# Kernel tuning notes

Hardware: AMD Instinct MI355X
Metric: run time of the kernel (lower is better)

The kernel has to match this reference:

```python
import jax, jax.numpy as jnp
import numpy as np

N_ATOMS = 10000
N_EDGES = 200000
L_MAX = 2
K_L = [32, 24, 16]  # k_max_l = n_element_channels * n_max_l

# (l1, l2, L) in the original loop order (l1 outer, l2 inner, L ascending)
PAIRS = [(0,0,0),(0,1,1),(0,2,2),
         (1,0,1),(1,1,0),(1,1,1),(1,1,2),(1,2,1),(1,2,2),
         (2,0,2),(2,1,1),(2,1,2),(2,2,0),(2,2,1),(2,2,2)]
# concatenated input width -> k_max_l[L] per (L, sigma) channel
LIN = {'0_1': (72, 32), '1_1': (80, 24), '1_m1': (40, 24), '2_1': (72, 16), '2_m1': (32, 16)}


def setup_inputs() -> dict:
    key = jax.random.key(0)
    it = iter(jax.random.split(key, 64))
    def nrm(shape):
        return jax.random.normal(next(it), shape, dtype=jnp.float32)
    inp = {}
    for l in range(L_MAX + 1):
        inp['rb%d' % l] = nrm((N_EDGES, K_L[l]))           # radial basis per l
    for l in range(L_MAX + 1):
        inp['sh%d' % l] = nrm((N_EDGES, 2*l+1, 1))         # spherical harmonics per l
    inp['emb'] = nrm((N_ATOMS, 1, K_L[0]))                 # initial center embedding
    for l in range(L_MAX + 1):
        inp['f%d' % l] = nrm((N_ATOMS, 2*l+1, K_L[l]))     # nu=1 equivariant features
    for (l1, l2, L) in PAIRS:
        inp['cg_%d_%d_%d' % (l1, l2, L)] = nrm(((2*l1+1)*(2*l2+1), 2*L+1))
    for LS, (fin, fout) in LIN.items():
        inp['W_' + LS] = nrm((fin, fout)) / np.float32(np.sqrt(fin))
        inp['b_' + LS] = nrm((fout,)) * 0.01
    inp['centers'] = jax.random.randint(next(it), (N_EDGES,), 0, N_ATOMS)
    inp['neighbors'] = jax.random.randint(next(it), (N_EDGES,), 0, N_ATOMS)
    inp['n_atoms'] = N_ATOMS
    return inp


def _normalize(x, dims):
    # Normalizer(dims): RMS normalization over the given dims
    return x * jax.lax.rsqrt(jnp.mean(x * x, axis=dims, keepdims=True) + 1e-12)


def _forward(floats, centers, neighbors, n_atoms):
    (rb0, rb1, rb2, sh0, sh1, sh2, emb, f0, f1, f2,
     cg_0_0_0, cg_0_1_1, cg_0_2_2, cg_1_0_1, cg_1_1_0, cg_1_1_1, cg_1_1_2,
     cg_1_2_1, cg_1_2_2, cg_2_0_2, cg_2_1_1, cg_2_1_2, cg_2_2_0, cg_2_2_1,
     cg_2_2_2, W_0_1, b_0_1, W_1_1, b_1_1, W_1_m1, b_1_m1, W_2_1, b_2_1,
     W_2_m1, b_2_m1) = floats
    rb = [rb0, rb1, rb2]; sh = [sh0, sh1, sh2]; feats = [f0, f1, f2]
    cgs = {'0_0_0': cg_0_0_0, '0_1_1': cg_0_1_1, '0_2_2': cg_0_2_2,
           '1_0_1': cg_1_0_1, '1_1_0': cg_1_1_0, '1_1_1': cg_1_1_1,
           '1_1_2': cg_1_1_2, '1_2_1': cg_1_2_1, '1_2_2': cg_1_2_2,
           '2_0_2': cg_2_0_2, '2_1_1': cg_2_1_1, '2_1_2': cg_2_1_2,
           '2_2_0': cg_2_2_0, '2_2_1': cg_2_2_1, '2_2_2': cg_2_2_2}
    lin = {'0_1': (W_0_1, b_0_1), '1_1': (W_1_1, b_1_1), '1_m1': (W_1_m1, b_1_m1),
           '2_1': (W_2_1, b_2_1), '2_m1': (W_2_m1, b_2_m1)}

    # ---- InvariantMessagePasser: density_l = scatter_add over centers of
    #      sh_l * rb_l * emb[neighbors]
    emb_n = emb[neighbors]                                       # [E, 1, k0]
    densities = []
    for l in range(L_MAX + 1):
        msg = sh[l] * rb[l][:, None, :] * emb_n[:, :, :K_L[l]]   # [E, 2l+1, k_l]
        densities.append(jax.ops.segment_sum(msg, centers, num_segments=n_atoms))

    # ---- EquivariantMessagePasser
    ve = [sh[l] * rb[l][:, None, :] for l in range(L_MAX + 1)]   # vector expansion [E,2l+1,k_l]
    fn = [feats[l][neighbors] for l in range(L_MAX + 1)]         # gathered neighbor feats
    results = {}
    for (l1, l2, L) in PAIRS:
        S = (-1) ** (l1 + l2 + L)
        k = min(K_L[l1], K_L[l2])
        t1 = ve[l1][:, :, :k]                                    # [E, 2l1+1, k]
        t2 = fn[l2][:, :, :k]                                    # [E, 2l2+1, k]
        cg = cgs['%d_%d_%d' % (l1, l2, L)].reshape(2*l1+1, 2*l2+1, 2*L+1)
        # fused outer product + CG contraction -> [E, 2L+1, k]
        res = jnp.einsum('eak,ebk,abM->eMk', t1, t2, cg)
        pooled = jax.ops.segment_sum(res, centers, num_segments=n_atoms)
        LS = '%d_%s' % (L, 'm1' if S < 0 else '1')
        results.setdefault(LS, []).append(pooled)

    outs = {}
    for LS, (W, b) in lin.items():
        x = jnp.concatenate(results[LS], axis=2)                 # [n_atoms, 2L+1, size_LS]
        x = _normalize(x, (0, 1))
        x = jnp.einsum('amf,fk->amk', x, W) + b
        outs[LS] = _normalize(x, (0, 1, 2))

    return (densities[0], densities[1], densities[2],
            outs['0_1'], outs['1_1'], outs['1_m1'], outs['2_1'], outs['2_m1'])


def reference(rb0, rb1, rb2, sh0, sh1, sh2, emb, f0, f1, f2,
              cg_0_0_0, cg_0_1_1, cg_0_2_2, cg_1_0_1, cg_1_1_0, cg_1_1_1,
              cg_1_1_2, cg_1_2_1, cg_1_2_2, cg_2_0_2, cg_2_1_1, cg_2_1_2,
              cg_2_2_0, cg_2_2_1, cg_2_2_2, W_0_1, b_0_1, W_1_1, b_1_1,
              W_1_m1, b_1_m1, W_2_1, b_2_1, W_2_m1, b_2_m1,
              centers, neighbors, n_atoms):
    floats = (rb0, rb1, rb2, sh0, sh1, sh2, emb, f0, f1, f2,
              cg_0_0_0, cg_0_1_1, cg_0_2_2, cg_1_0_1, cg_1_1_0, cg_1_1_1,
              cg_1_1_2, cg_1_2_1, cg_1_2_2, cg_2_0_2, cg_2_1_1, cg_2_1_2,
              cg_2_2_0, cg_2_2_1, cg_2_2_2, W_0_1, b_0_1, W_1_1, b_1_1,
              W_1_m1, b_1_m1, W_2_1, b_2_1, W_2_m1, b_2_m1)
    return _forward(floats, centers, neighbors, n_atoms)
```

## Files before the change

### kernel.cpp

```cpp
#include <hip/hip_runtime.h>
#include <hip/hip_bf16.h>

typedef __hip_bfloat16 bf16;

#define N_ATOMS 10000
#define N_EDGES 200000

#define SCG   0
#define SINV  616
#define SS1P  1024
#define SS2P  19968
#define SWS2  20288
#define SINTS 20352
#define IFLAG  0
#define ICOUNT 16
#define IOFFS  10016
#define ICURS  20032
#define IELIST 30032
#define INTS_END_SMALL 230032
#define INTS_END_BIG   430032
#define SXACC (SINTS + INTS_END_BIG)
#define BIG_FLOATS (SXACC + 952*N_ATOMS)

#define O0 0
#define O1 320000
#define O2 1040000
#define OY 1840000

__device__ __forceinline__ float b2f(bf16 x){ return __bfloat162float(x); }
__device__ __forceinline__ bf16  f2b(float x){ return __float2bfloat16(x); }

__device__ __forceinline__ float ldv(const float* p, int i){ return p[i]; }
__device__ __forceinline__ float ldv(const bf16*  p, int i){ return b2f(p[i]); }
__device__ __forceinline__ void  stv(float* p, int i, float v){ p[i] = v; }
__device__ __forceinline__ void  stv(bf16*  p, int i, float v){ p[i] = f2b(v); }

template<typename T> __device__ __forceinline__ int dtid();
template<> __device__ __forceinline__ int dtid<bf16>(){ return 0; }
template<> __device__ __forceinline__ int dtid<float>(){ return 1; }

struct Ptrs15 { const void* p[15]; };
struct LinP   { const void* W[5]; const void* B[5]; };

__constant__ int c_cg_sizes[15] = {1,9,25,9,9,27,45,45,75,25,45,75,25,75,125};
__constant__ int c_fin[5]   = {72,80,40,72,32};
__constant__ int c_kout[5]  = {32,24,24,16,16};
__constant__ int c_yoff[5]  = {OY+0, OY+320000, OY+1040000, OY+1760000, OY+2560000};
__constant__ int c_numel[5] = {320000,720000,720000,800000,800000};
__constant__ int c_cum[6]   = {0,32,104,176,256,336};
__constant__ int c_xb[5]    = {0,72,312,432,792};
__constant__ int c_Ms[5]    = {1,3,3,5,5};

__global__ void k_probe(const unsigned short* rb0u, const unsigned short* embu,
                        int* flag) {
  int lane = threadIdx.x;
  int bad = 0;
  for (int i = lane; i < 256; i += 64) {
    unsigned u1 = ((unsigned)rb0u[2*i]) << 16;
    unsigned u2 = ((unsigned)embu[2*i]) << 16;
    float v1 = __uint_as_float(u1);
    float v2 = __uint_as_float(u2);
    if (!(fabsf(v1) < 1e9f) || !(fabsf(v2) < 1e9f)) bad = 1;
  }
  unsigned long long any = __ballot(bad);
  if (lane == 0) flag[0] = (any != 0ULL) ? 1 : 0;
}

__global__ void k_zero(float* wsf, int* wsi) {
  int i = blockIdx.x*blockDim.x + threadIdx.x;
  if (i < N_ATOMS) wsi[ICOUNT + i] = 0;
  int j = i - N_ATOMS;
  if (j >= 0 && j < N_ATOMS) wsi[ICURS + j] = 0;
  j -= N_ATOMS;
  if (j >= 0 && j < 18944) wsf[SS1P + j] = 0.f;
  j -= 18944;
  if (j >= 0 && j < 325) wsf[SS2P + j] = 0.f;
}

template<typename T>
__global__ void k_cg(Ptrs15 cg, float* wsf, const int* flag) {
  if (flag[0] != dtid<T>()) return;
  int i = blockIdx.x*blockDim.x + threadIdx.x;
  if (i >= 615) return;
  int s = 0, off = i;
  while (off >= c_cg_sizes[s]) { off -= c_cg_sizes[s]; ++s; }
  wsf[SCG + i] = ldv((const T*)cg.p[s], off);
}

__global__ void k_hist(const int* __restrict__ centers, int* __restrict__ counts) {
  int e = blockIdx.x*blockDim.x + threadIdx.x;
  if (e < N_EDGES) atomicAdd(&counts[centers[e]], 1);
}

__global__ void k_scan(const int* __restrict__ counts, int* __restrict__ offs) {
  __shared__ int part[1024];
  int t = threadIdx.x;
  int base = t*10;
  int s = 0;
  for (int i = 0; i < 10; ++i) { int idx = base+i; if (idx < N_ATOMS) s += counts[idx]; }
  part[t] = s;
  __syncthreads();
  for (int d = 1; d < 1024; d <<= 1) {
    int v = part[t];
    int add = (t >= d) ? part[t-d] : 0;
    __syncthreads();
    part[t] = v + add;
    __syncthreads();
  }
  int run = (t == 0) ? 0 : part[t-1];
  for (int i = 0; i < 10; ++i) {
    int idx = base+i;
    if (idx < N_ATOMS) { offs[idx] = run; run += counts[idx]; }
  }
  if (t == 1023) offs[N_ATOMS] = part[1023];
}

__global__ void k_scatter(const int* __restrict__ centers, const int* __restrict__ offs,
                          int* __restrict__ cursors, int* __restrict__ elist) {
  int e = blockIdx.x*blockDim.x + threadIdx.x;
  if (e < N_EDGES) {
    int c = centers[e];
    int p = atomicAdd(&cursors[c], 1);
    elist[offs[c] + p] = e;
  }
}

__global__ void k_scatter2(const int* __restrict__ centers, const int* __restrict__ neighbors,
                           const int* __restrict__ offs, int* __restrict__ cursors,
                           int2* __restrict__ elist2) {
  int e = blockIdx.x*blockDim.x + threadIdx.x;
  if (e < N_EDGES) {
    int c = centers[e];
    int p = atomicAdd(&cursors[c], 1);
    elist2[offs[c] + p] = make_int2(e, neighbors[e]);
  }
}

template<typename T, int MODE>
__global__ __launch_bounds__(256) void k_main(
    const T* __restrict__ rb0, const T* __restrict__ rb1, const T* __restrict__ rb2,
    const T* __restrict__ sh0, const T* __restrict__ sh1, const T* __restrict__ sh2,
    const T* __restrict__ emb, const T* __restrict__ f0, const T* __restrict__ f1,
    const T* __restrict__ f2, const int* __restrict__ neighbors,
    const int* __restrict__ offs, const int* __restrict__ elist,
    const float* __restrict__ cgf, float* __restrict__ s1p,
    const float* __restrict__ inv, float* __restrict__ s2p,
    float* __restrict__ xout, LinP lp, T* __restrict__ out,
    const int* __restrict__ flag)
{
  if (flag[0] != dtid<T>()) return;
  int lane = threadIdx.x & 63;
  int wv   = threadIdx.x >> 6;
  int a = blockIdx.x;
  int beg = offs[a];
  int cnt = offs[a+1] - beg;
  int k32 = lane & 31, e2 = lane >> 5;
  int k16 = lane & 15, e4 = lane >> 4;
  const int2* el2 = (const int2*)elist;
  int ab = a & 63;

  __shared__ float L[952];
  __shared__ float red[4][5];

  float acc[20];
  #pragma unroll
  for (int i = 0; i < 20; ++i) acc[i] = 0.f;

  if (wv == 0) {
    const float* C000 = cgf + 0;
    const float* C011 = cgf + 1;
    const float* C101 = cgf + 35;
    const float* C110 = cgf + 44;
    const float* C111 = cgf + 53;
    const float* C112 = cgf + 80;
    for (int base = 0; base < cnt; base += 2) {
      int idx = base + e2;
      if (idx < cnt) {
        int e, n;
        if constexpr (MODE == 0) { int2 en = el2[beg + idx]; e = en.x; n = en.y; }
        else { e = elist[beg + idx]; n = neighbors[e]; }
        float s0 = ldv(sh0, e);
        float s1a0 = ldv(sh1, e*3+0), s1a1 = ldv(sh1, e*3+1), s1a2 = ldv(sh1, e*3+2);
        float rb0k = ldv(rb0, e*32 + k32);
        float ek   = ldv(emb, n*32 + k32);
        float f0k  = ldv(f0,  n*32 + k32);
        float ve0 = s0 * rb0k;
        acc[0] = fmaf(ve0, ek, acc[0]);
        acc[4] = fmaf(C000[0]*ve0, f0k, acc[4]);
        if (k32 < 24) {
          float rb1k = ldv(rb1, e*24 + k32);
          float f1k0 = ldv(f1, n*72 + k32);
          float f1k1 = ldv(f1, n*72 + 24 + k32);
          float f1k2 = ldv(f1, n*72 + 48 + k32);
          float rbek = rb1k * ek;
          acc[1] = fmaf(s1a0, rbek, acc[1]);
          acc[2] = fmaf(s1a1, rbek, acc[2]);
          acc[3] = fmaf(s1a2, rbek, acc[3]);
          #pragma unroll
          for (int bb = 0; bb < 3; ++bb) {
            float fb = (bb==0)?f1k0:(bb==1)?f1k1:f1k2;
            float p = ve0 * fb;
            #pragma unroll
            for (int M = 0; M < 3; ++M) acc[5+M] = fmaf(p, C011[bb*3+M], acc[5+M]);
          }
          float g3 = rb1k * f0k;
          #pragma unroll
          for (int aa = 0; aa < 3; ++aa) {
            float sa = (aa==0)?s1a0:(aa==1)?s1a1:s1a2;
            float p = g3 * sa;
            #pragma unroll
            for (int M = 0; M < 3; ++M) acc[8+M] = fmaf(p, C101[aa*3+M], acc[8+M]);
          }
          #pragma unroll
          for (int aa = 0; aa < 3; ++aa) {
            float sa = rb1k * ((aa==0)?s1a0:(aa==1)?s1a1:s1a2);
            #pragma unroll
            for (int bb = 0; bb < 3; ++bb) {
              float fb = (bb==0)?f1k0:(bb==1)?f1k1:f1k2;
              float p = sa * fb;
              int q = aa*3+bb;
              acc[11] = fmaf(p, C110[q], acc[11]);
              #pragma unroll
              for (int M = 0; M < 3; ++M) acc[12+M] = fmaf(p, C111[q*3+M], acc[12+M]);
              #pragma unroll
              for (int M = 0; M < 5; ++M) acc[15+M] = fmaf(p, C112[q*5+M], acc[15+M]);
            }
          }
        }
      }
    }
    #pragma unroll
    for (int i = 0; i < 20; ++i) acc[i] += __shfl_xor(acc[i], 32);
  } else if (wv == 1) {
    const float* C022 = cgf + 10;
    const float* C121 = cgf + 125;
    const float* C122 = cgf + 170;
    for (int base = 0; base < cnt; base += 4) {
      int idx = base + e4;
      if (idx < cnt) {
        int e, n;
        if constexpr (MODE == 0) { int2 en = el2[beg + idx]; e = en.x; n = en.y; }
        else { e = elist[beg + idx]; n = neighbors[e]; }
        float s0 = ldv(sh0, e);
        float s1a[3];
        #pragma unroll
        for (int m = 0; m < 3; ++m) s1a[m] = ldv(sh1, e*3+m);
        float s2a[5];
        #pragma unroll
        for (int m = 0; m < 5; ++m) s2a[m] = ldv(sh2, e*5+m);
        float rb0k = ldv(rb0, e*32 + k16);
        float rb1k = ldv(rb1, e*24 + k16);
        float rb2k = ldv(rb2, e*16 + k16);
        float ek   = ldv(emb, n*32 + k16);
        float f2k[5];
        #pragma unroll
        for (int b = 0; b < 5; ++b) f2k[b] = ldv(f2, n*80 + b*16 + k16);
        float re = rb2k * ek;
        #pragma unroll
        for (int m = 0; m < 5; ++m) acc[m] = fmaf(s2a[m], re, acc[m]);
        float ve0 = s0 * rb0k;
        #pragma unroll
        for (int bb = 0; bb < 5; ++bb) {
          float p = ve0 * f2k[bb];
          #pragma unroll
          for (int M = 0; M < 5; ++M) acc[5+M] = fmaf(p, C022[bb*5+M], acc[5+M]);
        }
        #pragma unroll
        for (int aa = 0; aa < 3; ++aa) {
          float sa = rb1k * s1a[aa];
          #pragma unroll
          for (int bb = 0; bb < 5; ++bb) {
            float p = sa * f2k[bb];
            int q = aa*5+bb;
            #pragma unroll
            for (int M = 0; M < 3; ++M) acc[10+M] = fmaf(p, C121[q*3+M], acc[10+M]);
            #pragma unroll
            for (int M = 0; M < 5; ++M) acc[13+M] = fmaf(p, C122[q*5+M], acc[13+M]);
          }
        }
      }
    }
    #pragma unroll
    for (int i = 0; i < 18; ++i) {
      acc[i] += __shfl_xor(acc[i], 16);
      acc[i] += __shfl_xor(acc[i], 32);
    }
  } else if (wv == 2) {
    const float* C202 = cgf + 245;
    const float* C211 = cgf + 270;
    const float* C212 = cgf + 315;
    for (int base = 0; base < cnt; base += 4) {
      int idx = base + e4;
      if (idx < cnt) {
        int e, n;
        if constexpr (MODE == 0) { int2 en = el2[beg + idx]; e = en.x; n = en.y; }
        else { e = elist[beg + idx]; n = neighbors[e]; }
        float s2a[5];
        #pragma unroll
        for (int m = 0; m < 5; ++m) s2a[m] = ldv(sh2, e*5+m);
        float rb2k = ldv(rb2, e*16 + k16);
        float f0k  = ldv(f0,  n*32 + k16);
        float f1k[3];
        #pragma unroll
        for (int b = 0; b < 3; ++b) f1k[b] = ldv(f1, n*72 + b*24 + k16);
        float g9 = rb2k * f0k;
        #pragma unroll
        for (int aa = 0; aa < 5; ++aa) {
          float p = g9 * s2a[aa];
          #pragma unroll
          for (int M = 0; M < 5; ++M) acc[0+M] = fmaf(p, C202[aa*5+M], acc[0+M]);
        }
        #pragma unroll
        for (int aa = 0; aa < 5; ++aa) {
          float sa = rb2k * s2a[aa];
          #pragma unroll
          for (int bb = 0; bb < 3; ++bb) {
            float p = sa * f1k[bb];
            int q = aa*3+bb;
            #pragma unroll
            for (int M = 0; M < 3; ++M) acc[5+M] = fmaf(p, C211[q*3+M], acc[5+M]);
            #pragma unroll
            for (int M = 0; M < 5; ++M) acc[8+M] = fmaf(p, C212[q*5+M], acc[8+M]);
          }
        }
      }
    }
    #pragma unroll
    for (int i = 0; i < 13; ++i) {
      acc[i] += __shfl_xor(acc[i], 16);
      acc[i] += __shfl_xor(acc[i], 32);
    }
  } else {
    const float* C220 = cgf + 390;
    const float* C221 = cgf + 415;
    const float* C222 = cgf + 490;
    for (int base = 0; base < cnt; base += 4) {
      int idx = base + e4;
      if (idx < cnt) {
        int e, n;
        if constexpr (MODE == 0) { int2 en = el2[beg + idx]; e = en.x; n = en.y; }
        else { e = elist[beg + idx]; n = neighbors[e]; }
        float s2a[5];
        #pragma unroll
        for (int m = 0; m < 5; ++m) s2a[m] = ldv(sh2, e*5+m);
        float rb2k = ldv(rb2, e*16 + k16);
        float f2k[5];
        #pragma unroll
        for (int b = 0; b < 5; ++b) f2k[b] = ldv(f2, n*80 + b*16 + k16);
        #pragma unroll
        for (int aa = 0; aa < 5; ++aa) {
          float sa = rb2k * s2a[aa];
          #pragma unroll
          for (int bb = 0; bb < 5; ++bb) {
            float p = sa * f2k[bb];
            int q = aa*5+bb;
            acc[0] = fmaf(p, C220[q], acc[0]);
            #pragma unroll
            for (int M = 0; M < 3; ++M) acc[1+M] = fmaf(p, C221[q*3+M], acc[1+M]);
            #pragma unroll
            for (int M = 0; M < 5; ++M) acc[4+M] = fmaf(p, C222[q*5+M], acc[4+M]);
          }
        }
      }
    }
    #pragma unroll
    for (int i = 0; i < 9; ++i) {
      acc[i] += __shfl_xor(acc[i], 16);
      acc[i] += __shfl_xor(acc[i], 32);
    }
  }

  if constexpr (MODE != 2) {
    if (wv == 0) {
      if (lane < 32) {
        stv(out, O0 + a*32 + k32, acc[0]);
        atomicAdd(&s1p[(0+k32)*64+ab], acc[4]*acc[4]);
        if (k32 < 24) {
          #pragma unroll
          for (int m = 0; m < 3; ++m) stv(out, O1 + a*72 + m*24 + k32, acc[1+m]);
          atomicAdd(&s1p[(32+k32)*64+ab], acc[11]*acc[11]);
          float q;
          q = acc[5]*acc[5]+acc[6]*acc[6]+acc[7]*acc[7];
          atomicAdd(&s1p[(72+k32)*64+ab], q);
          q = acc[8]*acc[8]+acc[9]*acc[9]+acc[10]*acc[10];
          atomicAdd(&s1p[(96+k32)*64+ab], q);
          q = acc[12]*acc[12]+acc[13]*acc[13]+acc[14]*acc[14];
          atomicAdd(&s1p[(152+k32)*64+ab], q);
          q = acc[15]*acc[15]+acc[16]*acc[16]+acc[17]*acc[17]
            + acc[18]*acc[18]+acc[19]*acc[19];
          atomicAdd(&s1p[(208+k32)*64+ab], q);
        }
      }
    } else if (wv == 1) {
      if (lane < 16) {
        #pragma unroll
        for (int m = 0; m < 5; ++m) stv(out, O2 + a*80 + m*16 + k16, acc[m]);
        float q;
        q = acc[5]*acc[5]+acc[6]*acc[6]+acc[7]*acc[7]+acc[8]*acc[8]+acc[9]*acc[9];
        atomicAdd(&s1p[(192+k16)*64+ab], q);
        q = acc[10]*acc[10]+acc[11]*acc[11]+acc[12]*acc[12];
        atomicAdd(&s1p[(120+k16)*64+ab], q);
        q = acc[13]*acc[13]+acc[14]*acc[14]+acc[15]*acc[15]
          + acc[16]*acc[16]+acc[17]*acc[17];
        atomicAdd(&s1p[(264+k16)*64+ab], q);
      }
    } else if (wv == 2) {
      if (lane < 16) {
        float q;
        q = acc[0]*acc[0]+acc[1]*acc[1]+acc[2]*acc[2]+acc[3]*acc[3]+acc[4]*acc[4];
        atomicAdd(&s1p[(232+k16)*64+ab], q);
        q = acc[5]*acc[5]+acc[6]*acc[6]+acc[7]*acc[7];
        atomicAdd(&s1p[(136+k16)*64+ab], q);
        q = acc[8]*acc[8]+acc[9]*acc[9]+acc[10]*acc[10]
          + acc[11]*acc[11]+acc[12]*acc[12];
        atomicAdd(&s1p[(280+k16)*64+ab], q);
      }
    } else {
      if (lane < 16) {
        atomicAdd(&s1p[(56+k16)*64+ab], acc[0]*acc[0]);
        float q;
        q = acc[1]*acc[1]+acc[2]*acc[2]+acc[3]*acc[3];
        atomicAdd(&s1p[(176+k16)*64+ab], q);
        q = acc[4]*acc[4]+acc[5]*acc[5]+acc[6]*acc[6]
          + acc[7]*acc[7]+acc[8]*acc[8];
        atomicAdd(&s1p[(248+k16)*64+ab], q);
      }
    }
  }

  if constexpr (MODE == 0) {
    float* xg = xout + a*952;
    if (wv == 0) {
      if (lane < 32) {
        xg[k32] = acc[4];
        if (k32 < 24) {
          xg[32+k32] = acc[11];
          #pragma unroll
          for (int M = 0; M < 3; ++M) xg[72+M*80+k32]     = acc[5+M];
          #pragma unroll
          for (int M = 0; M < 3; ++M) xg[72+M*80+24+k32]  = acc[8+M];
          #pragma unroll
          for (int M = 0; M < 3; ++M) xg[312+M*40+k32]    = acc[12+M];
          #pragma unroll
          for (int M = 0; M < 5; ++M) xg[432+M*72+16+k32] = acc[15+M];
        }
      }
    } else if (wv == 1) {
      if (lane < 16) {
        #pragma unroll
        for (int M = 0; M < 5; ++M) xg[432+M*72+k16]    = acc[5+M];
        #pragma unroll
        for (int M = 0; M < 3; ++M) xg[72+M*80+48+k16]  = acc[10+M];
        #pragma unroll
        for (int M = 0; M < 5; ++M) xg[792+M*32+k16]    = acc[13+M];
      }
    } else if (wv == 2) {
      if (lane < 16) {
        #pragma unroll
        for (int M = 0; M < 5; ++M) xg[432+M*72+40+k16] = acc[0+M];
        #pragma unroll
        for (int M = 0; M < 3; ++M) xg[72+M*80+64+k16]  = acc[5+M];
        #pragma unroll
        for (int M = 0; M < 5; ++M) xg[792+M*32+16+k16] = acc[8+M];
      }
    } else {
      if (lane < 16) {
        xg[56+k16] = acc[0];
        #pragma unroll
        for (int M = 0; M < 3; ++M) xg[312+M*40+24+k16] = acc[1+M];
        #pragma unroll
        for (int M = 0; M < 5; ++M) xg[432+M*72+56+k16] = acc[4+M];
      }
    }
  }

  if constexpr (MODE == 2) {
    if (wv == 0) {
      if (lane < 32) {
        L[k32] = acc[4]*inv[k32];
        if (k32 < 24) {
          L[32+k32] = acc[11]*inv[32+k32];
          #pragma unroll
          for (int M = 0; M < 3; ++M) L[72+M*80+k32]     = acc[5+M]*inv[72+k32];
          #pragma unroll
          for (int M = 0; M < 3; ++M) L[72+M*80+24+k32]  = acc[8+M]*inv[96+k32];
          #pragma unroll
          for (int M = 0; M < 3; ++M) L[312+M*40+k32]    = acc[12+M]*inv[152+k32];
          #pragma unroll
          for (int M = 0; M < 5; ++M) L[432+M*72+16+k32] = acc[15+M]*inv[208+k32];
        }
      }
    } else if (wv == 1) {
      if (lane < 16) {
        #pragma unroll
        for (int M = 0; M < 5; ++M) L[432+M*72+k16]    = acc[5+M]*inv[192+k16];
        #pragma unroll
        for (int M = 0; M < 3; ++M) L[72+M*80+48+k16]  = acc[10+M]*inv[120+k16];
        #pragma unroll
        for (int M = 0; M < 5; ++M) L[792+M*32+k16]    = acc[13+M]*inv[264+k16];
      }
    } else if (wv == 2) {
      if (lane < 16) {
        #pragma unroll
        for (int M = 0; M < 5; ++M) L[432+M*72+40+k16] = acc[0+M]*inv[232+k16];
        #pragma unroll
        for (int M = 0; M < 3; ++M) L[72+M*80+64+k16]  = acc[5+M]*inv[136+k16];
        #pragma unroll
        for (int M = 0; M < 5; ++M) L[792+M*32+16+k16] = acc[8+M]*inv[280+k16];
      }
    } else {
      if (lane < 16) {
        L[56+k16] = acc[0]*inv[56+k16];
        #pragma unroll
        for (int M = 0; M < 3; ++M) L[312+M*40+24+k16] = acc[1+M]*inv[176+k16];
        #pragma unroll
        for (int M = 0; M < 5; ++M) L[432+M*72+56+k16] = acc[4+M]*inv[248+k16];
      }
    }
    __syncthreads();
    int t = threadIdx.x;
    float y2[5] = {0.f,0.f,0.f,0.f,0.f};
    for (int tau = t; tau < 336; tau += 256) {
      int ls = 0;
      while (tau >= c_cum[ls+1]) ++ls;
      int rem = tau - c_cum[ls];
      int kn = c_kout[ls], fin = c_fin[ls];
      int M = rem / kn, ko = rem - M*kn;
      const T* W = (const T*)lp.W[ls];
      float y = ldv((const T*)lp.B[ls], ko);
      const float* xv = &L[c_xb[ls] + M*fin];
      for (int f = 0; f < fin; ++f) y = fmaf(xv[f], ldv(W, f*kn+ko), y);
      stv(out, c_yoff[ls] + (a*c_Ms[ls] + M)*kn + ko, y);
      y2[ls] += y*y;
    }
    #pragma unroll
    for (int i = 0; i < 5; ++i) {
      y2[i] += __shfl_xor(y2[i], 1);  y2[i] += __shfl_xor(y2[i], 2);
      y2[i] += __shfl_xor(y2[i], 4);  y2[i] += __shfl_xor(y2[i], 8);
      y2[i] += __shfl_xor(y2[i], 16); y2[i] += __shfl_xor(y2[i], 32);
    }
    if (lane == 0) {
      #pragma unroll
      for (int i = 0; i < 5; ++i) red[wv][i] = y2[i];
    }
    __syncthreads();
    if (t == 0) {
      #pragma unroll
      for (int i = 0; i < 5; ++i)
        atomicAdd(&s2p[i*64 + ab], red[0][i]+red[1][i]+red[2][i]+red[3][i]);
    }
  }
}

template<typename T>
__global__ __launch_bounds__(256) void k_lin(
    const float* __restrict__ xg, const float* __restrict__ inv,
    LinP lp, T* __restrict__ out, float* __restrict__ s2p,
    const int* __restrict__ flag)
{
  if (flag[0] != dtid<T>()) return;
  int a = blockIdx.x;
  int t = threadIdx.x;
  __shared__ float L[952];
  for (int i = t; i < 952; i += 256) {
    int ch;
    if      (i < 72)  ch = i;
    else if (i < 312) ch = 72  + (i-72)  % 80;
    else if (i < 432) ch = 152 + (i-312) % 40;
    else if (i < 792) ch = 192 + (i-432) % 72;
    else              ch = 264 + (i-792) % 32;
    L[i] = xg[a*952 + i] * inv[ch];
  }
  __syncthreads();
  float y2[5] = {0.f,0.f,0.f,0.f,0.f};
  for (int tau = t; tau < 336; tau += 256) {
    int ls = 0;
    while (tau >= c_cum[ls+1]) ++ls;
    int rem = tau - c_cum[ls];
    int kn = c_kout[ls], fin = c_fin[ls];
    int M = rem / kn, ko = rem - M*kn;
    const T* W = (const T*)lp.W[ls];
    float y = ldv((const T*)lp.B[ls], ko);
    const float* xv = &L[c_xb[ls] + M*fin];
    for (int f = 0; f < fin; ++f) y = fmaf(xv[f], ldv(W, f*kn+ko), y);
    stv(out, c_yoff[ls] + (a*c_Ms[ls] + M)*kn + ko, y);
    y2[ls] += y*y;
  }
  __shared__ float red[4][5];
  #pragma unroll
  for (int i = 0; i < 5; ++i) {
    y2[i] += __shfl_xor(y2[i], 1);  y2[i] += __shfl_xor(y2[i], 2);
    y2[i] += __shfl_xor(y2[i], 4);  y2[i] += __shfl_xor(y2[i], 8);
    y2[i] += __shfl_xor(y2[i], 16); y2[i] += __shfl_xor(y2[i], 32);
  }
  if ((t & 63) == 0) {
    #pragma unroll
    for (int i = 0; i < 5; ++i) red[t>>6][i] = y2[i];
  }
  __syncthreads();
  if (t == 0) {
    #pragma unroll
    for (int i = 0; i < 5; ++i)
      atomicAdd(&s2p[i*64 + (a & 63)], red[0][i]+red[1][i]+red[2][i]+red[3][i]);
  }
}

__global__ void k_red1(const float* __restrict__ s1p, float* __restrict__ inv) {
  int ch = blockIdx.x, lane = threadIdx.x;
  float v = s1p[ch*64 + lane];
  v += __shfl_xor(v, 1);  v += __shfl_xor(v, 2);  v += __shfl_xor(v, 4);
  v += __shfl_xor(v, 8);  v += __shfl_xor(v, 16); v += __shfl_xor(v, 32);
  if (lane == 0) {
    float rows = (ch < 72) ? 10000.f : (ch < 192) ? 30000.f : 50000.f;
    inv[ch] = rsqrtf(v/rows + 1e-12f);
  }
}

__global__ void k_red2(const float* __restrict__ s2p, float* __restrict__ ws2) {
  int ls = blockIdx.x, lane = threadIdx.x;
  float v = s2p[ls*64 + lane];
  v += __shfl_xor(v, 1);  v += __shfl_xor(v, 2);  v += __shfl_xor(v, 4);
  v += __shfl_xor(v, 8);  v += __shfl_xor(v, 16); v += __shfl_xor(v, 32);
  if (lane == 0) ws2[ls] = v;
}

template<typename T>
__global__ void k_scale(const float* __restrict__ ws2, T* __restrict__ out,
                        const int* __restrict__ flag) {
  if (flag[0] != dtid<T>()) return;
  int i = blockIdx.x*blockDim.x + threadIdx.x;
  if (i >= 3360000) return;
  int ls = (i < 320000) ? 0 : (i < 1040000) ? 1 : (i < 1760000) ? 2 : (i < 2560000) ? 3 : 4;
  float scale = rsqrtf(ws2[ls] / (float)c_numel[ls] + 1e-12f);
  stv(out, OY + i, ldv((const T*)out, OY + i) * scale);
}

template<typename T>
static void launch_chain(void* const* d_in, T* out, float* wsf, int* wsi,
                         Ptrs15 cg, LinP lp, bool big, hipStream_t stream) {
  const T* rb0 = (const T*)d_in[0];
  const T* rb1 = (const T*)d_in[1];
  const T* rb2 = (const T*)d_in[2];
  const T* sh0 = (const T*)d_in[3];
  const T* sh1 = (const T*)d_in[4];
  const T* sh2 = (const T*)d_in[5];
  const T* emb = (const T*)d_in[6];
  const T* f0  = (const T*)d_in[7];
  const T* f1  = (const T*)d_in[8];
  const T* f2  = (const T*)d_in[9];
  const int* neighbors = (const int*)d_in[36];
  const int* flag = wsi + IFLAG;

  k_cg<T><<<3, 256, 0, stream>>>(cg, wsf, flag);
  if (big) {
    k_main<T,0><<<N_ATOMS, 256, 0, stream>>>(rb0, rb1, rb2, sh0, sh1, sh2, emb, f0, f1, f2,
        neighbors, wsi+IOFFS, wsi+IELIST, wsf+SCG, wsf+SS1P, nullptr, nullptr,
        wsf+SXACC, lp, out, flag);
    k_red1<<<296, 64, 0, stream>>>(wsf+SS1P, wsf+SINV);
    k_lin<T><<<N_ATOMS, 256, 0, stream>>>(wsf+SXACC, wsf+SINV, lp, out, wsf+SS2P, flag);
  } else {
    k_main<T,1><<<N_ATOMS, 256, 0, stream>>>(rb0, rb1, rb2, sh0, sh1, sh2, emb, f0, f1, f2,
        neighbors, wsi+IOFFS, wsi+IELIST, wsf+SCG, wsf+SS1P, nullptr, nullptr,
        nullptr, lp, out, flag);
    k_red1<<<296, 64, 0, stream>>>(wsf+SS1P, wsf+SINV);
    k_main<T,2><<<N_ATOMS, 256, 0, stream>>>(rb0, rb1, rb2, sh0, sh1, sh2, emb, f0, f1, f2,
        neighbors, wsi+IOFFS, wsi+IELIST, wsf+SCG, nullptr, wsf+SINV, wsf+SS2P,
        nullptr, lp, out, flag);
  }
  k_red2<<<5, 64, 0, stream>>>(wsf+SS2P, wsf+SWS2);
  k_scale<T><<<(3360000+255)/256, 256, 0, stream>>>(wsf+SWS2, out, flag);
}

extern "C" void kernel_launch(void* const* d_in, const int* in_sizes, int n_in,
                              void* d_out, int out_size, void* d_ws, size_t ws_size,
                              hipStream_t stream) {
  float* wsf = (float*)d_ws;
  int*   wsi = (int*)(wsf + SINTS);
  const int* centers   = (const int*)d_in[35];
  const int* neighbors = (const int*)d_in[36];
  bool big = ws_size >= (size_t)BIG_FLOATS * 4;

  Ptrs15 cg;
  for (int i = 0; i < 15; ++i) cg.p[i] = d_in[10+i];
  LinP lp;
  lp.W[0] = d_in[25]; lp.B[0] = d_in[26];
  lp.W[1] = d_in[27]; lp.B[1] = d_in[28];
  lp.W[2] = d_in[29]; lp.B[2] = d_in[30];
  lp.W[3] = d_in[31]; lp.B[3] = d_in[32];
  lp.W[4] = d_in[33]; lp.B[4] = d_in[34];

  k_probe<<<1, 64, 0, stream>>>((const unsigned short*)d_in[0],
                                (const unsigned short*)d_in[6], wsi + IFLAG);
  k_zero<<<154, 256, 0, stream>>>(wsf, wsi);
  k_hist<<<(N_EDGES+255)/256, 256, 0, stream>>>(centers, wsi+ICOUNT);
  k_scan<<<1, 1024, 0, stream>>>(wsi+ICOUNT, wsi+IOFFS);
  if (big) {
    k_scatter2<<<(N_EDGES+255)/256, 256, 0, stream>>>(centers, neighbors, wsi+IOFFS,
                                                      wsi+ICURS, (int2*)(wsi+IELIST));
  } else {
    k_scatter<<<(N_EDGES+255)/256, 256, 0, stream>>>(centers, wsi+IOFFS, wsi+ICURS, wsi+IELIST);
  }

  launch_chain<bf16 >(d_in, (bf16*)d_out,  wsf, wsi, cg, lp, big, stream);
  launch_chain<float>(d_in, (float*)d_out, wsf, wsi, cg, lp, big, stream);
}
```

Before: 517.4 us.

## Stage edge lists in LDS, fuse probe into zero kernel, skip unused dtype chain

Merges the dtype probe into the zeroing kernel, which removes one launch. Each block now loads chunks of 256 (edge, neighbor) pairs into shared memory once, and all four waves read from there instead of each gathering them from global memory. Wave 0 unrolls two edges per iteration with masked weights, and MODE 0 writes its output through LDS with coalesced float4 stores. On the host, the input byte size decides which dtype chain to launch, so the unused chain's launches are skipped. The risk is that the host-side dtype detection depends on in_sizes being filled in.

Result: no change. 511.5 us (-1.1%).

```diff
diff --git a/kernel.cpp b/kernel.cpp
--- a/kernel.cpp
+++ b/kernel.cpp
@@ -51,22 +51,21 @@
 __constant__ int c_xb[5]    = {0,72,312,432,792};
 __constant__ int c_Ms[5]    = {1,3,3,5,5};
 
-__global__ void k_probe(const unsigned short* rb0u, const unsigned short* embu,
-                        int* flag) {
-  int lane = threadIdx.x;
-  int bad = 0;
-  for (int i = lane; i < 256; i += 64) {
-    unsigned u1 = ((unsigned)rb0u[2*i]) << 16;
-    unsigned u2 = ((unsigned)embu[2*i]) << 16;
-    float v1 = __uint_as_float(u1);
-    float v2 = __uint_as_float(u2);
-    if (!(fabsf(v1) < 1e9f) || !(fabsf(v2) < 1e9f)) bad = 1;
-  }
-  unsigned long long any = __ballot(bad);
-  if (lane == 0) flag[0] = (any != 0ULL) ? 1 : 0;
-}
-
-__global__ void k_zero(float* wsf, int* wsi) {
+__global__ void k_zero(float* wsf, int* wsi,
+                       const unsigned short* rb0u, const unsigned short* embu) {
+  if (blockIdx.x == 0 && threadIdx.x < 64) {
+    int lane = threadIdx.x;
+    int bad = 0;
+    for (int i = lane; i < 256; i += 64) {
+      unsigned u1 = ((unsigned)rb0u[2*i]) << 16;
+      unsigned u2 = ((unsigned)embu[2*i]) << 16;
+      float v1 = __uint_as_float(u1);
+      float v2 = __uint_as_float(u2);
+      if (!(fabsf(v1) < 1e9f) || !(fabsf(v2) < 1e9f)) bad = 1;
+    }
+    unsigned long long any = __ballot(bad);
+    if (lane == 0) wsi[IFLAG] = (any != 0ULL) ? 1 : 0;
+  }
   int i = blockIdx.x*blockDim.x + threadIdx.x;
   if (i < N_ATOMS) wsi[ICOUNT + i] = 0;
   int j = i - N_ATOMS;
@@ -151,6 +150,7 @@
   if (flag[0] != dtid<T>()) return;
   int lane = threadIdx.x & 63;
   int wv   = threadIdx.x >> 6;
+  int tix  = threadIdx.x;
   int a = blockIdx.x;
   int beg = offs[a];
   int cnt = offs[a+1] - beg;
@@ -159,210 +159,230 @@
   const int2* el2 = (const int2*)elist;
   int ab = a & 63;
 
-  __shared__ float L[952];
+  __shared__ int2 sel[256];
+  __shared__ __align__(16) float L[952];
   __shared__ float red[4][5];
 
   float acc[20];
   #pragma unroll
   for (int i = 0; i < 20; ++i) acc[i] = 0.f;
 
-  if (wv == 0) {
-    const float* C000 = cgf + 0;
-    const float* C011 = cgf + 1;
-    const float* C101 = cgf + 35;
-    const float* C110 = cgf + 44;
-    const float* C111 = cgf + 53;
-    const float* C112 = cgf + 80;
-    for (int base = 0; base < cnt; base += 2) {
-      int idx = base + e2;
-      if (idx < cnt) {
-        int e, n;
-        if constexpr (MODE == 0) { int2 en = el2[beg + idx]; e = en.x; n = en.y; }
-        else { e = elist[beg + idx]; n = neighbors[e]; }
-        float s0 = ldv(sh0, e);
-        float s1a0 = ldv(sh1, e*3+0), s1a1 = ldv(sh1, e*3+1), s1a2 = ldv(sh1, e*3+2);
-        float rb0k = ldv(rb0, e*32 + k32);
-        float ek   = ldv(emb, n*32 + k32);
-        float f0k  = ldv(f0,  n*32 + k32);
-        float ve0 = s0 * rb0k;
-        acc[0] = fmaf(ve0, ek, acc[0]);
-        acc[4] = fmaf(C000[0]*ve0, f0k, acc[4]);
-        if (k32 < 24) {
-          float rb1k = ldv(rb1, e*24 + k32);
-          float f1k0 = ldv(f1, n*72 + k32);
-          float f1k1 = ldv(f1, n*72 + 24 + k32);
-          float f1k2 = ldv(f1, n*72 + 48 + k32);
-          float rbek = rb1k * ek;
-          acc[1] = fmaf(s1a0, rbek, acc[1]);
-          acc[2] = fmaf(s1a1, rbek, acc[2]);
-          acc[3] = fmaf(s1a2, rbek, acc[3]);
-          #pragma unroll
-          for (int bb = 0; bb < 3; ++bb) {
-            float fb = (bb==0)?f1k0:(bb==1)?f1k1:f1k2;
-            float p = ve0 * fb;
-            #pragma unroll
-            for (int M = 0; M < 3; ++M) acc[5+M] = fmaf(p, C011[bb*3+M], acc[5+M]);
-          }
-          float g3 = rb1k * f0k;
-          #pragma unroll
-          for (int aa = 0; aa < 3; ++aa) {
-            float sa = (aa==0)?s1a0:(aa==1)?s1a1:s1a2;
-            float p = g3 * sa;
-            #pragma unroll
-            for (int M = 0; M < 3; ++M) acc[8+M] = fmaf(p, C101[aa*3+M], acc[8+M]);
-          }
-          #pragma unroll
-          for (int aa = 0; aa < 3; ++aa) {
-            float sa = rb1k * ((aa==0)?s1a0:(aa==1)?s1a1:s1a2);
+  for (int cbase = 0; cbase < cnt; cbase += 256) {
+    int nch = cnt - cbase; if (nch > 256) nch = 256;
+    __syncthreads();
+    if (tix < nch) {
+      if constexpr (MODE == 0) {
+        sel[tix] = el2[beg + cbase + tix];
+      } else {
+        int e = elist[beg + cbase + tix];
+        sel[tix] = make_int2(e, neighbors[e]);
+      }
+    }
+    __syncthreads();
+
+    if (wv == 0) {
+      const float* C000 = cgf + 0;
+      const float* C011 = cgf + 1;
+      const float* C101 = cgf + 35;
+      const float* C110 = cgf + 44;
+      const float* C111 = cgf + 53;
+      const float* C112 = cgf + 80;
+      for (int base = 0; base < nch; base += 4) {
+        #pragma unroll
+        for (int u = 0; u < 2; ++u) {
+          int idx = base + 2*u + e2;
+          float w = (idx < nch) ? 1.f : 0.f;
+          int ic  = (idx < nch) ? idx : (nch - 1);
+          int2 en = sel[ic];
+          int e = en.x, n = en.y;
+          float s0 = ldv(sh0, e);
+          float s1a0 = ldv(sh1, e*3+0), s1a1 = ldv(sh1, e*3+1), s1a2 = ldv(sh1, e*3+2);
+          float rb0k = ldv(rb0, e*32 + k32) * w;
+          float ek   = ldv(emb, n*32 + k32);
+          float f0k  = ldv(f0,  n*32 + k32);
+          float ve0 = s0 * rb0k;
+          acc[0] = fmaf(ve0, ek, acc[0]);
+          acc[4] = fmaf(C000[0]*ve0, f0k, acc[4]);
+          if (k32 < 24) {
+            float rb1k = ldv(rb1, e*24 + k32) * w;
+            float f1k0 = ldv(f1, n*72 + k32);
+            float f1k1 = ldv(f1, n*72 + 24 + k32);
+            float f1k2 = ldv(f1, n*72 + 48 + k32);
+            float rbek = rb1k * ek;
+            acc[1] = fmaf(s1a0, rbek, acc[1]);
+            acc[2] = fmaf(s1a1, rbek, acc[2]);
+            acc[3] = fmaf(s1a2, rbek, acc[3]);
             #pragma unroll
             for (int bb = 0; bb < 3; ++bb) {
               float fb = (bb==0)?f1k0:(bb==1)?f1k1:f1k2;
-              float p = sa * fb;
-              int q = aa*3+bb;
-              acc[11] = fmaf(p, C110[q], acc[11]);
-              #pragma unroll
-              for (int M = 0; M < 3; ++M) acc[12+M] = fmaf(p, C111[q*3+M], acc[12+M]);
-              #pragma unroll
-              for (int M = 0; M < 5; ++M) acc[15+M] = fmaf(p, C112[q*5+M], acc[15+M]);
+              float p = ve0 * fb;
+              #pragma unroll
+              for (int M = 0; M < 3; ++M) acc[5+M] = fmaf(p, C011[bb*3+M], acc[5+M]);
+            }
+            float g3 = rb1k * f0k;
+            #pragma unroll
+            for (int aa = 0; aa < 3; ++aa) {
+              float sa = (aa==0)?s1a0:(aa==1)?s1a1:s1a2;
+              float p = g3 * sa;
+              #pragma unroll
+              for (int M = 0; M < 3; ++M) acc[8+M] = fmaf(p, C101[aa*3+M], acc[8+M]);
+            }
+            #pragma unroll
+            for (int aa = 0; aa < 3; ++aa) {
+              float sa = rb1k * ((aa==0)?s1a0:(aa==1)?s1a1:s1a2);
+              #pragma unroll
+              for (int bb = 0; bb < 3; ++bb) {
+                float fb = (bb==0)?f1k0:(bb==1)?f1k1:f1k2;
+                float p = sa * fb;
+                int q = aa*3+bb;
+                acc[11] = fmaf(p, C110[q], acc[11]);
+                #pragma unroll
+                for (int M = 0; M < 3; ++M) acc[12+M] = fmaf(p, C111[q*3+M], acc[12+M]);
+                #pragma unroll
+                for (int M = 0; M < 5; ++M) acc[15+M] = fmaf(p, C112[q*5+M], acc[15+M]);
+              }
             }
           }
         }
       }
-    }
+    } else if (wv == 1) {
+      const float* C022 = cgf + 10;
+      const float* C121 = cgf + 125;
+      const float* C122 = cgf + 170;
+      for (int base = 0; base < nch; base += 4) {
+        int idx = base + e4;
+        if (idx < nch) {
+          int2 en = sel[idx];
+          int e = en.x, n = en.y;
+          float s0 = ldv(sh0, e);
+          float s1a[3];
+          #pragma unroll
+          for (int m = 0; m < 3; ++m) s1a[m] = ldv(sh1, e*3+m);
+          float s2a[5];
+          #pragma unroll
+          for (int m = 0; m < 5; ++m) s2a[m] = ldv(sh2, e*5+m);
+          float rb0k = ldv(rb0, e*32 + k16);
+          float rb1k = ldv(rb1, e*24 + k16);
+          float rb2k = ldv(rb2, e*16 + k16);
+          float ek   = ldv(emb, n*32 + k16);
+          float f2k[5];
+          #pragma unroll
+          for (int b = 0; b < 5; ++b) f2k[b] = ldv(f2, n*80 + b*16 + k16);
+          float re = rb2k * ek;
+          #pragma unroll
+          for (int m = 0; m < 5; ++m) acc[m] = fmaf(s2a[m], re, acc[m]);
+          float ve0 = s0 * rb0k;
+          #pragma unroll
+          for (int bb = 0; bb < 5; ++bb) {
+            float p = ve0 * f2k[bb];
+            #pragma unroll
+            for (int M = 0; M < 5; ++M) acc[5+M] = fmaf(p, C022[bb*5+M], acc[5+M]);
+          }
+          #pragma unroll
+          for (int aa = 0; aa < 3; ++aa) {
+            float sa = rb1k * s1a[aa];
+            #pragma unroll
+            for (int bb = 0; bb < 5; ++bb) {
+              float p = sa * f2k[bb];
+              int q = aa*5+bb;
+              #pragma unroll
+              for (int M = 0; M < 3; ++M) acc[10+M] = fmaf(p, C121[q*3+M], acc[10+M]);
+              #pragma unroll
+              for (int M = 0; M < 5; ++M) acc[13+M] = fmaf(p, C122[q*5+M], acc[13+M]);
+            }
+          }
+        }
+      }
+    } else if (wv == 2) {
+      const float* C202 = cgf + 245;
+      const float* C211 = cgf + 270;
+      const float* C212 = cgf + 315;
+      for (int base = 0; base < nch; base += 4) {
+        int idx = base + e4;
+        if (idx < nch) {
+          int2 en = sel[idx];
+          int e = en.x, n = en.y;
+          float s2a[5];
+          #pragma unroll
+          for (int m = 0; m < 5; ++m) s2a[m] = ldv(sh2, e*5+m);
+          float rb2k = ldv(rb2, e*16 + k16);
+          float f0k  = ldv(f0,  n*32 + k16);
+          float f1k[3];
+          #pragma unroll
+          for (int b = 0; b < 3; ++b) f1k[b] = ldv(f1, n*72 + b*24 + k16);
+          float g9 = rb2k * f0k;
+          #pragma unroll
+          for (int aa = 0; aa < 5; ++aa) {
+            float p = g9 * s2a[aa];
+            #pragma unroll
+            for (int M = 0; M < 5; ++M) acc[0+M] = fmaf(p, C202[aa*5+M], acc[0+M]);
+          }
+          #pragma unroll
+          for (int aa = 0; aa < 5; ++aa) {
+            float sa = rb2k * s2a[aa];
+            #pragma unroll
+            for (int bb = 0; bb < 3; ++bb) {
+              float p = sa * f1k[bb];
+              int q = aa*3+bb;
+              #pragma unroll
+              for (int M = 0; M < 3; ++M) acc[5+M] = fmaf(p, C211[q*3+M], acc[5+M]);
+              #pragma unroll
+              for (int M = 0; M < 5; ++M) acc[8+M] = fmaf(p, C212[q*5+M], acc[8+M]);
+            }
+          }
+        }
+      }
+    } else {
+      const float* C220 = cgf + 390;
+      const float* C221 = cgf + 415;
+      const float* C222 = cgf + 490;
+      for (int base = 0; base < nch; base += 4) {
+        int idx = base + e4;
+        if (idx < nch) {
+          int2 en = sel[idx];
+          int e = en.x, n = en.y;
+          float s2a[5];
+          #pragma unroll
+          for (int m = 0; m < 5; ++m) s2a[m] = ldv(sh2, e*5+m);
+          float rb2k = ldv(rb2, e*16 + k16);
+          float f2k[5];
+          #pragma unroll
+          for (int b = 0; b < 5; ++b) f2k[b] = ldv(f2, n*80 + b*16 + k16);
+          #pragma unroll
+          for (int aa = 0; aa < 5; ++aa) {
+            float sa = rb2k * s2a[aa];
+            #pragma unroll
+            for (int bb = 0; bb < 5; ++bb) {
+              float p = sa * f2k[bb];
+              int q = aa*5+bb;
+              acc[0] = fmaf(p, C220[q], acc[0]);
+              #pragma unroll
+              for (int M = 0; M < 3; ++M) acc[1+M] = fmaf(p, C221[q*3+M], acc[1+M]);
+              #pragma unroll
+              for (int M = 0; M < 5; ++M) acc[4+M] = fmaf(p, C222[q*5+M], acc[4+M]);
+            }
+          }
+        }
+      }
+    }
+  }
+
+  if (wv == 0) {
     #pragma unroll
     for (int i = 0; i < 20; ++i) acc[i] += __shfl_xor(acc[i], 32);
   } else if (wv == 1) {
-    const float* C022 = cgf + 10;
-    const float* C121 = cgf + 125;
-    const float* C122 = cgf + 170;
-    for (int base = 0; base < cnt; base += 4) {
-      int idx = base + e4;
-      if (idx < cnt) {
-        int e, n;
-        if constexpr (MODE == 0) { int2 en = el2[beg + idx]; e = en.x; n = en.y; }
-        else { e = elist[beg + idx]; n = neighbors[e]; }
-        float s0 = ldv(sh0, e);
-        float s1a[3];
-        #pragma unroll
-        for (int m = 0; m < 3; ++m) s1a[m] = ldv(sh1, e*3+m);
-        float s2a[5];
-        #pragma unroll
-        for (int m = 0; m < 5; ++m) s2a[m] = ldv(sh2, e*5+m);
-        float rb0k = ldv(rb0, e*32 + k16);
-        float rb1k = ldv(rb1, e*24 + k16);
-        float rb2k = ldv(rb2, e*16 + k16);
-        float ek   = ldv(emb, n*32 + k16);
-        float f2k[5];
-        #pragma unroll
-        for (int b = 0; b < 5; ++b) f2k[b] = ldv(f2, n*80 + b*16 + k16);
-        float re = rb2k * ek;
-        #pragma unroll
-        for (int m = 0; m < 5; ++m) acc[m] = fmaf(s2a[m], re, acc[m]);
-        float ve0 = s0 * rb0k;
-        #pragma unroll
-        for (int bb = 0; bb < 5; ++bb) {
-          float p = ve0 * f2k[bb];
-          #pragma unroll
-          for (int M = 0; M < 5; ++M) acc[5+M] = fmaf(p, C022[bb*5+M], acc[5+M]);
-        }
-        #pragma unroll
-        for (int aa = 0; aa < 3; ++aa) {
-          float sa = rb1k * s1a[aa];
-          #pragma unroll
-          for (int bb = 0; bb < 5; ++bb) {
-            float p = sa * f2k[bb];
-            int q = aa*5+bb;
-            #pragma unroll
-            for (int M = 0; M < 3; ++M) acc[10+M] = fmaf(p, C121[q*3+M], acc[10+M]);
-            #pragma unroll
-            for (int M = 0; M < 5; ++M) acc[13+M] = fmaf(p, C122[q*5+M], acc[13+M]);
-          }
-        }
-      }
-    }
     #pragma unroll
     for (int i = 0; i < 18; ++i) {
       acc[i] += __shfl_xor(acc[i], 16);
       acc[i] += __shfl_xor(acc[i], 32);
     }
   } else if (wv == 2) {
-    const float* C202 = cgf + 245;
-    const float* C211 = cgf + 270;
-    const float* C212 = cgf + 315;
-    for (int base = 0; base < cnt; base += 4) {
-      int idx = base + e4;
-      if (idx < cnt) {
-        int e, n;
-        if constexpr (MODE == 0) { int2 en = el2[beg + idx]; e = en.x; n = en.y; }
-        else { e = elist[beg + idx]; n = neighbors[e]; }
-        float s2a[5];
-        #pragma unroll
-        for (int m = 0; m < 5; ++m) s2a[m] = ldv(sh2, e*5+m);
-        float rb2k = ldv(rb2, e*16 + k16);
-        float f0k  = ldv(f0,  n*32 + k16);
-        float f1k[3];
-        #pragma unroll
-        for (int b = 0; b < 3; ++b) f1k[b] = ldv(f1, n*72 + b*24 + k16);
-        float g9 = rb2k * f0k;
-        #pragma unroll
-        for (int aa = 0; aa < 5; ++aa) {
-          float p = g9 * s2a[aa];
-          #pragma unroll
-          for (int M = 0; M < 5; ++M) acc[0+M] = fmaf(p, C202[aa*5+M], acc[0+M]);
-        }
-        #pragma unroll
-        for (int aa = 0; aa < 5; ++aa) {
-          float sa = rb2k * s2a[aa];
-          #pragma unroll
-          for (int bb = 0; bb < 3; ++bb) {
-            float p = sa * f1k[bb];
-            int q = aa*3+bb;
-            #pragma unroll
-            for (int M = 0; M < 3; ++M) acc[5+M] = fmaf(p, C211[q*3+M], acc[5+M]);
-            #pragma unroll
-            for (int M = 0; M < 5; ++M) acc[8+M] = fmaf(p, C212[q*5+M], acc[8+M]);
-          }
-        }
-      }
-    }
     #pragma unroll
     for (int i = 0; i < 13; ++i) {
       acc[i] += __shfl_xor(acc[i], 16);
       acc[i] += __shfl_xor(acc[i], 32);
     }
   } else {
-    const float* C220 = cgf + 390;
-    const float* C221 = cgf + 415;
-    const float* C222 = cgf + 490;
-    for (int base = 0; base < cnt; base += 4) {
-      int idx = base + e4;
-      if (idx < cnt) {
-        int e, n;
-        if constexpr (MODE == 0) { int2 en = el2[beg + idx]; e = en.x; n = en.y; }
-        else { e = elist[beg + idx]; n = neighbors[e]; }
-        float s2a[5];
-        #pragma unroll
-        for (int m = 0; m < 5; ++m) s2a[m] = ldv(sh2, e*5+m);
-        float rb2k = ldv(rb2, e*16 + k16);
-        float f2k[5];
-        #pragma unroll
-        for (int b = 0; b < 5; ++b) f2k[b] = ldv(f2, n*80 + b*16 + k16);
-        #pragma unroll
-        for (int aa = 0; aa < 5; ++aa) {
-          float sa = rb2k * s2a[aa];
-          #pragma unroll
-          for (int bb = 0; bb < 5; ++bb) {
-            float p = sa * f2k[bb];
-            int q = aa*5+bb;
-            acc[0] = fmaf(p, C220[q], acc[0]);
-            #pragma unroll
-            for (int M = 0; M < 3; ++M) acc[1+M] = fmaf(p, C221[q*3+M], acc[1+M]);
-            #pragma unroll
-            for (int M = 0; M < 5; ++M) acc[4+M] = fmaf(p, C222[q*5+M], acc[4+M]);
-          }
-        }
-      }
-    }
     #pragma unroll
     for (int i = 0; i < 9; ++i) {
       acc[i] += __shfl_xor(acc[i], 16);
@@ -429,49 +449,52 @@
   }
 
   if constexpr (MODE == 0) {
-    float* xg = xout + a*952;
     if (wv == 0) {
       if (lane < 32) {
-        xg[k32] = acc[4];
+        L[k32] = acc[4];
         if (k32 < 24) {
-          xg[32+k32] = acc[11];
-          #pragma unroll
-          for (int M = 0; M < 3; ++M) xg[72+M*80+k32]     = acc[5+M];
-          #pragma unroll
-          for (int M = 0; M < 3; ++M) xg[72+M*80+24+k32]  = acc[8+M];
-          #pragma unroll
-          for (int M = 0; M < 3; ++M) xg[312+M*40+k32]    = acc[12+M];
-          #pragma unroll
-          for (int M = 0; M < 5; ++M) xg[432+M*72+16+k32] = acc[15+M];
+          L[32+k32] = acc[11];
+          #pragma unroll
+          for (int M = 0; M < 3; ++M) L[72+M*80+k32]     = acc[5+M];
+          #pragma unroll
+          for (int M = 0; M < 3; ++M) L[72+M*80+24+k32]  = acc[8+M];
+          #pragma unroll
+          for (int M = 0; M < 3; ++M) L[312+M*40+k32]    = acc[12+M];
+          #pragma unroll
+          for (int M = 0; M < 5; ++M) L[432+M*72+16+k32] = acc[15+M];
         }
       }
     } else if (wv == 1) {
       if (lane < 16) {
         #pragma unroll
-        for (int M = 0; M < 5; ++M) xg[432+M*72+k16]    = acc[5+M];
-        #pragma unroll
-        for (int M = 0; M < 3; ++M) xg[72+M*80+48+k16]  = acc[10+M];
-        #pragma unroll
-        for (int M = 0; M < 5; ++M) xg[792+M*32+k16]    = acc[13+M];
+        for (int M = 0; M < 5; ++M) L[432+M*72+k16]    = acc[5+M];
+        #pragma unroll
+        for (int M = 0; M < 3; ++M) L[72+M*80+48+k16]  = acc[10+M];
+        #pragma unroll
+        for (int M = 0; M < 5; ++M) L[792+M*32+k16]    = acc[13+M];
       }
     } else if (wv == 2) {
       if (lane < 16) {
         #pragma unroll
-        for (int M = 0; M < 5; ++M) xg[432+M*72+40+k16] = acc[0+M];
-        #pragma unroll
-        for (int M = 0; M < 3; ++M) xg[72+M*80+64+k16]  = acc[5+M];
-        #pragma unroll
-        for (int M = 0; M < 5; ++M) xg[792+M*32+16+k16] = acc[8+M];
+        for (int M = 0; M < 5; ++M) L[432+M*72+40+k16] = acc[0+M];
+        #pragma unroll
+        for (int M = 0; M < 3; ++M) L[72+M*80+64+k16]  = acc[5+M];
+        #pragma unroll
+        for (int M = 0; M < 5; ++M) L[792+M*32+16+k16] = acc[8+M];
       }
     } else {
       if (lane < 16) {
-        xg[56+k16] = acc[0];
-        #pragma unroll
-        for (int M = 0; M < 3; ++M) xg[312+M*40+24+k16] = acc[1+M];
-        #pragma unroll
-        for (int M = 0; M < 5; ++M) xg[432+M*72+56+k16] = acc[4+M];
-      }
-    }
+        L[56+k16] = acc[0];
+        #pragma unroll
+        for (int M = 0; M < 3; ++M) L[312+M*40+24+k16] = acc[1+M];
+        #pragma unroll
+        for (int M = 0; M < 5; ++M) L[432+M*72+56+k16] = acc[4+M];
+      }
+    }
+    __syncthreads();
+    const float4* Ls = (const float4*)L;
+    float4* xd = (float4*)(xout + a*952);
+    for (int i = tix; i < 238; i += 256) xd[i] = Ls[i];
   }
 
   if constexpr (MODE == 2) {
@@ -680,6 +703,13 @@
   const int* neighbors = (const int*)d_in[36];
   bool big = ws_size >= (size_t)BIG_FLOATS * 4;
 
+  int know = -1;
+  if (in_sizes) {
+    long long nb = (long long)in_sizes[0];
+    if (nb == (long long)N_EDGES*32*2) know = 0;
+    else if (nb == (long long)N_EDGES*32*4) know = 1;
+  }
+
   Ptrs15 cg;
   for (int i = 0; i < 15; ++i) cg.p[i] = d_in[10+i];
   LinP lp;
@@ -689,9 +719,9 @@
   lp.W[3] = d_in[31]; lp.B[3] = d_in[32];
   lp.W[4] = d_in[33]; lp.B[4] = d_in[34];
 
-  k_probe<<<1, 64, 0, stream>>>((const unsigned short*)d_in[0],
-                                (const unsigned short*)d_in[6], wsi + IFLAG);
-  k_zero<<<154, 256, 0, stream>>>(wsf, wsi);
+  k_zero<<<154, 256, 0, stream>>>(wsf, wsi,
+                                  (const unsigned short*)d_in[0],
+                                  (const unsigned short*)d_in[6]);
   k_hist<<<(N_EDGES+255)/256, 256, 0, stream>>>(centers, wsi+ICOUNT);
   k_scan<<<1, 1024, 0, stream>>>(wsi+ICOUNT, wsi+IOFFS);
   if (big) {
@@ -701,6 +731,6 @@
     k_scatter<<<(N_EDGES+255)/256, 256, 0, stream>>>(centers, wsi+IOFFS, wsi+ICURS, wsi+IELIST);
   }
 
-  launch_chain<bf16 >(d_in, (bf16*)d_out,  wsf, wsi, cg, lp, big, stream);
-  launch_chain<float>(d_in, (float*)d_out, wsf, wsi, cg, lp, big, stream);
-}
+  if (know != 1) launch_chain<bf16 >(d_in, (bf16*)d_out,  wsf, wsi, cg, lp, big, stream);
+  if (know != 0) launch_chain<float>(d_in, (float*)d_out, wsf, wsi, cg, lp, big, stream);
+}
```
